# Kernel optimization log

Hardware: AMD Instinct MI355X
Metric: run time of the kernel (lower is better)

The kernel has to match this reference:

```python
import jax, jax.numpy as jnp
import numpy as np

B, D, E, H, K = 8192, 1024, 8, 4096, 2

def setup_inputs() -> dict:
    key = jax.random.key(0)
    ks = jax.random.split(key, 7)
    s_in = 1.0 / np.sqrt(D)
    s_hid = 1.0 / np.sqrt(H)
    return {
        "z":  jax.random.normal(ks[0], (B, D), dtype=jnp.float32),
        "Wg": jax.random.uniform(ks[1], (D, E), jnp.float32, -s_in, s_in),
        "bg": jnp.zeros((E,), jnp.float32),
        "W1": jax.random.uniform(ks[2], (E, D, H), jnp.float32, -s_in, s_in),
        "b1": jax.random.uniform(ks[3], (E, H), jnp.float32, -s_in, s_in),
        "W2": jax.random.uniform(ks[4], (E, H, D), jnp.float32, -s_hid, s_hid),
        "b2": jax.random.uniform(ks[5], (E, D), jnp.float32, -s_hid, s_hid),
    }

def reference(z, Wg, bg, W1, b1, W2, b2):
    # gate: softmax over experts, then keep only top-k weights (no renorm,
    # matching the original which sums topw * expert(z))
    w = jax.nn.softmax(z @ Wg + bg, axis=-1)            # [B, E]
    topw, idx = jax.lax.top_k(w, K)                      # [B, K] each
    wmask = jnp.zeros_like(w).at[jnp.arange(B)[:, None], idx].set(topw)  # [B, E]
    # dense all-expert MLP, then weighted combine (same math as per-token loop)
    h = jax.nn.relu(jnp.einsum('bd,edh->beh', z, W1) + b1)   # [B, E, H]
    y = jnp.einsum('beh,ehd->bed', h, W2) + b2               # [B, E, D]
    out = jnp.einsum('be,bed->bd', wmask, y)                 # [B, D]
    return out
```

## Files before the change

### kernel.cpp

```cpp
#include <hip/hip_runtime.h>
#include <hip/hip_bf16.h>
#include <cstdint>
#include <cstddef>

#define BTOK  8192
#define DIM   1024
#define NEXP  8
#define NHID  4096
#define HHALF 2048
#define GATE_TOK 64
#define ABASE (128 * 32)

typedef __bf16 bf16x8 __attribute__((ext_vector_type(8)));
typedef float  floatx4 __attribute__((ext_vector_type(4)));

#define O_COUNTS 0
#define O_BASE   256
#define O_TOKB   1024
#define O_TOKW   (O_TOKB + (size_t)NEXP*BTOK*4)
#define O_CE     (O_TOKW + (size_t)NEXP*BTOK*4)
#define O_CP     (O_CE + (size_t)2*BTOK*4)
#define O_CW     (O_CP + (size_t)2*BTOK*4)
#define O_ZBF    (O_CW + (size_t)2*BTOK*4)
#define O_W1T    (O_ZBF + (size_t)BTOK*DIM*2)
#define O_W2T    (O_W1T + (size_t)NEXP*DIM*NHID*2)
#define O_HBUF   (O_W2T + (size_t)NEXP*DIM*NHID*2)
#define WS_BASE  (O_HBUF + (size_t)2*BTOK*HHALF*2)
#define O_YBUF   WS_BASE
#define WS_FULL  (O_YBUF + (size_t)2*BTOK*DIM*4)

__device__ __forceinline__ void gload_lds16(const void* g, void* l) {
  __builtin_amdgcn_global_load_lds(
      (const __attribute__((address_space(1))) void*)g,
      (__attribute__((address_space(3))) void*)l, 16, 0, 0);
}

__device__ __forceinline__ ushort f2bf(float x) {
  return __builtin_bit_cast(ushort, __float2bfloat16(x));
}

__global__ void k_zcnt(int* __restrict__ counts) {
  if (threadIdx.x < 12) counts[threadIdx.x] = 0;
}

__global__ void k_zout(float* __restrict__ out) {
  int i = blockIdx.x * blockDim.x + threadIdx.x;
  float4 z4 = {0.f, 0.f, 0.f, 0.f};
  float4* o = (float4*)out;
  int n = BTOK * DIM / 4;
  for (int j = i; j < n; j += gridDim.x * blockDim.x) o[j] = z4;
}

__global__ __launch_bounds__(256) void k_transpose(
    const float* __restrict__ src, __hip_bfloat16* __restrict__ dst, int R, int C) {
  __shared__ float tile[32][33];
  int zz = blockIdx.z;
  const float* s = src + (size_t)zz * R * C;
  __hip_bfloat16* d = dst + (size_t)zz * R * C;
  int c0 = blockIdx.x * 32, r0 = blockIdx.y * 32;
  int tx = threadIdx.x & 31, ty = threadIdx.x >> 5;
#pragma unroll
  for (int i = ty; i < 32; i += 8)
    tile[i][tx] = s[(size_t)(r0 + i) * C + c0 + tx];
  __syncthreads();
#pragma unroll
  for (int i = ty; i < 32; i += 8)
    d[(size_t)(c0 + i) * R + r0 + tx] = __float2bfloat16(tile[tx][i]);
}

__global__ __launch_bounds__(256) void k_gate(
    const float* __restrict__ z, const float* __restrict__ Wg,
    const float* __restrict__ bg, int* __restrict__ counts,
    int* __restrict__ tokb, float* __restrict__ tokw,
    int* __restrict__ ce, int* __restrict__ cp, float* __restrict__ cw,
    __hip_bfloat16* __restrict__ zbf) {
  __shared__ float wgT[NEXP * DIM];
  __shared__ int   le[2 * GATE_TOK];
  __shared__ float lw[2 * GATE_TOK];
  __shared__ int   lr[2 * GATE_TOK];
  __shared__ int   lcnt[NEXP];
  __shared__ int   gbase[NEXP];

  int tid = threadIdx.x;
  if (tid < NEXP) lcnt[tid] = 0;
#pragma unroll
  for (int e = 0; e < NEXP; e++)
    for (int d = tid; d < DIM; d += 256)
      wgT[e * DIM + d] = Wg[d * NEXP + e];
  __syncthreads();

  int lane = tid & 63;
  int wv = tid >> 6;
  int b0 = blockIdx.x * GATE_TOK;

  for (int t = 0; t < 16; t++) {
    int lt = wv * 16 + t;
    int b = b0 + lt;
    const float4* zr4 = (const float4*)(z + (size_t)b * DIM);
    float4 zv[4];
#pragma unroll
    for (int i = 0; i < 4; i++) zv[i] = zr4[lane + 64 * i];
    ushort4* zb4 = (ushort4*)((ushort*)zbf + (size_t)b * DIM);
#pragma unroll
    for (int i = 0; i < 4; i++) {
      ushort4 u;
      u.x = f2bf(zv[i].x); u.y = f2bf(zv[i].y);
      u.z = f2bf(zv[i].z); u.w = f2bf(zv[i].w);
      zb4[lane + 64 * i] = u;
    }
    float acc[NEXP];
#pragma unroll
    for (int e = 0; e < NEXP; e++) acc[e] = 0.f;
#pragma unroll
    for (int e = 0; e < NEXP; e++) {
      const float4* wg4 = (const float4*)(wgT + e * DIM);
#pragma unroll
      for (int i = 0; i < 4; i++) {
        float4 w4 = wg4[lane + 64 * i];
        acc[e] += zv[i].x * w4.x + zv[i].y * w4.y + zv[i].z * w4.z + zv[i].w * w4.w;
      }
    }
#pragma unroll
    for (int off = 32; off > 0; off >>= 1) {
#pragma unroll
      for (int e = 0; e < NEXP; e++) acc[e] += __shfl_down(acc[e], off);
    }
    if (lane == 0) {
      float mx = -1e30f;
#pragma unroll
      for (int e = 0; e < NEXP; e++) { acc[e] += bg[e]; mx = fmaxf(mx, acc[e]); }
      float s = 0.f;
#pragma unroll
      for (int e = 0; e < NEXP; e++) { acc[e] = expf(acc[e] - mx); s += acc[e]; }
      float inv = 1.f / s;
      int i1 = -1, i2 = -1; float v1 = -1.f, v2 = -1.f;
#pragma unroll
      for (int e = 0; e < NEXP; e++) {
        float w = acc[e] * inv;
        if (w > v1) { v2 = v1; i2 = i1; v1 = w; i1 = e; }
        else if (w > v2) { v2 = w; i2 = e; }
      }
      le[2 * lt] = i1;     lw[2 * lt] = v1;
      le[2 * lt + 1] = i2; lw[2 * lt + 1] = v2;
    }
  }
  __syncthreads();
  if (tid < 2 * GATE_TOK) lr[tid] = atomicAdd(&lcnt[le[tid]], 1);
  __syncthreads();
  if (tid < NEXP) gbase[tid] = atomicAdd(&counts[tid], lcnt[tid]);
  __syncthreads();
  if (tid < 2 * GATE_TOK) {
    int e = le[tid];
    int p = gbase[e] + lr[tid];
    int b = b0 + (tid >> 1);
    int slot = tid & 1;
    tokb[e * BTOK + p] = b;
    tokw[e * BTOK + p] = lw[tid];
    ce[2 * b + slot] = e;
    cp[2 * b + slot] = p;
    cw[2 * b + slot] = lw[tid];
  }
}

__global__ void k_base(const int* __restrict__ counts, int* __restrict__ base) {
  if (threadIdx.x == 0 && blockIdx.x == 0) {
    int s = 0;
    for (int e = 0; e < NEXP; e++) { base[e] = s; s += counts[e]; }
    int a = 0, b = 0;
    base[8] = 0; base[17] = 0;
    for (int e = 0; e < NEXP; e++) {
      int mt = (counts[e] + 127) >> 7;
      a += mt * 8; b += mt * 4;
      base[9 + e] = a; base[18 + e] = b;
    }
  }
}


#define STG3(nxt_, tt_) do {                                                 \
    gload_lds16(srcA  + (tt_) * 32, &lds[nxt_][(wv * 16) * 32]);             \
    gload_lds16(srcB0 + (tt_) * 32, &lds[nxt_][ABASE + (wv * 16) * 32]);     \
    gload_lds16(srcB1 + (tt_) * 32, &lds[nxt_][ABASE + (128 + wv * 16) * 32]);\
  } while (0)

#define PH3(cur_, STG_, VM_) do {                                            \
    const ushort* Ab_ = &lds[cur_][0];                                       \
    const ushort* Bb_ = &lds[cur_][ABASE];                                   \
    bf16x8 afr_[4], bfr_[4];                                                 \
    _Pragma("unroll")                                                        \
    for (int j_ = 0; j_ < 4; j_++)                                           \
      bfr_[j_] = __builtin_bit_cast(bf16x8,                                  \
          *(const uint4*)(Bb_ + boff + j_ * 512));                           \
    _Pragma("unroll")                                                        \
    for (int i_ = 0; i_ < 4; i_++)                                           \
      afr_[i_] = __builtin_bit_cast(bf16x8,                                  \
          *(const uint4*)(Ab_ + aoff + i_ * 512));                           \
    STG_;                                                                    \
    __builtin_amdgcn_sched_barrier(0);                                       \
    VM_;                                                                     \
    __builtin_amdgcn_s_barrier();                                            \
    __builtin_amdgcn_sched_barrier(0);                                       \
    __builtin_amdgcn_s_setprio(1);                                           \
    _Pragma("unroll")                                                        \
    for (int i_ = 0; i_ < 4; i_++)                                           \
      _Pragma("unroll")                                                      \
      for (int j_ = 0; j_ < 4; j_++)                                         \
        acc[i_][j_] = __builtin_amdgcn_mfma_f32_16x16x32_bf16(               \
            afr_[i_], bfr_[j_], acc[i_][j_], 0, 0, 0);                       \
    __builtin_amdgcn_s_setprio(0);                                           \
    __builtin_amdgcn_sched_barrier(0);                                       \
    __builtin_amdgcn_s_barrier();                                            \
  } while (0)

#define VM3  asm volatile("s_waitcnt vmcnt(3)" ::: "memory")
#define VM0  asm volatile("s_waitcnt vmcnt(0)" ::: "memory")
#define NOP_ (void)0

__global__ __launch_bounds__(512, 4) void k_gemm1(
    const __hip_bfloat16* __restrict__ zbf, const __hip_bfloat16* __restrict__ w1t,
    const float* __restrict__ b1, const int* __restrict__ counts,
    const int* __restrict__ base, const int* __restrict__ tokb,
    __hip_bfloat16* __restrict__ hbuf, int hbase,
    const int* __restrict__ tp, int* __restrict__ steal) {
  __shared__ __align__(16) ushort lds[3][(128 + 256) * 32];
  __shared__ int sh_g;

  int tid = threadIdx.x;
  int lane = tid & 63;
  int wv = tid >> 6;
  int wm = wv >> 2;
  int wn = wv & 3;
  int lrow = lane & 15;
  int quad = lane >> 4;
  int pc = quad ^ ((lrow >> 1) & 3);
  int aoff = (wm * 64 + lrow) * 32 + pc * 8;
  int boff = (wn * 64 + lrow) * 32 + pc * 8;
  int srow = wv * 16 + (lane >> 2);
  int sswz = ((lane & 3) ^ ((srow >> 1) & 3)) * 8;

  const ushort* zb = (const ushort*)zbf;
  const ushort* w1 = (const ushort*)w1t;
  const int NT = DIM / 32;
  int TT = tp[8];

  for (;;) {
    if (tid == 0) sh_g = atomicAdd(steal, 1);
    __syncthreads();
    int g = sh_g;
    if (g >= TT) break;

    int e = 0;
    while (g >= tp[e + 1]) e++;
    int local = g - tp[e];
    int mte = (tp[e + 1] - tp[e]) >> 3;
    int nt = local / mte;
    int mtl = local - nt * mte;
    int m0 = mtl * 128, n0 = nt * 256;
    int cnt = counts[e], gb = base[e];

    int m = m0 + srow; if (m >= cnt) m = cnt - 1;
    const ushort* srcA = zb + (size_t)tokb[e * BTOK + m] * DIM + sswz;
    const ushort* srcB0 = w1 + (size_t)(e * NHID + hbase + n0 + srow) * DIM + sswz;
    const ushort* srcB1 = w1 + (size_t)(e * NHID + hbase + n0 + 128 + srow) * DIM + sswz;

    STG3(0, 0);
    STG3(1, 1);
    VM3;
    __builtin_amdgcn_s_barrier();

    floatx4 acc[4][4];
#pragma unroll
    for (int i = 0; i < 4; i++)
#pragma unroll
      for (int j = 0; j < 4; j++) { floatx4 zf = {0.f,0.f,0.f,0.f}; acc[i][j] = zf; }

    int cur = 0;
#pragma unroll 1
    for (int t = 0; t < NT - 2; ++t) {
      int nxt = cur + 2; if (nxt >= 3) nxt -= 3;
      PH3(cur, STG3(nxt, t + 2), VM3);
      cur = (cur == 2) ? 0 : cur + 1;
    }
    PH3(cur, NOP_, VM0);
    cur = (cur == 2) ? 0 : cur + 1;
    PH3(cur, NOP_, NOP_);

    float bias[4];
#pragma unroll
    for (int j = 0; j < 4; j++)
      bias[j] = b1[e * NHID + hbase + n0 + wn * 64 + j * 16 + lrow];
    ushort* hp = (ushort*)hbuf;
#pragma unroll
    for (int i = 0; i < 4; i++) {
      int mloc = wm * 64 + i * 16 + quad * 4;
#pragma unroll
      for (int r = 0; r < 4; r++) {
        int mm = m0 + mloc + r;
        if (mm < cnt) {
          ushort* hr = hp + (size_t)(gb + mm) * HHALF;
#pragma unroll
          for (int j = 0; j < 4; j++) {
            float v = fmaxf(acc[i][j][r] + bias[j], 0.f);
            hr[n0 + wn * 64 + j * 16 + lrow] = f2bf(v);
          }
        }
      }
    }
    __syncthreads();
  }
}

__global__ __launch_bounds__(512, 4) void k_gemm2(
    const __hip_bfloat16* __restrict__ hbuf, const __hip_bfloat16* __restrict__ w2t,
    const float* __restrict__ b2, const int* __restrict__ counts,
    const int* __restrict__ base, const int* __restrict__ tokb,
    const float* __restrict__ tokw, float* __restrict__ out,
    float* __restrict__ ybuf, int hbase, int pass,
    const int* __restrict__ tp, int* __restrict__ steal) {
  __shared__ __align__(16) ushort lds[3][(128 + 256) * 32];
  __shared__ int sh_g;

  int tid = threadIdx.x;
  int lane = tid & 63;
  int wv = tid >> 6;
  int wm = wv >> 2;
  int wn = wv & 3;
  int lrow = lane & 15;
  int quad = lane >> 4;
  int pc = quad ^ ((lrow >> 1) & 3);
  int aoff = (wm * 64 + lrow) * 32 + pc * 8;
  int boff = (wn * 64 + lrow) * 32 + pc * 8;
  int srow = wv * 16 + (lane >> 2);
  int sswz = ((lane & 3) ^ ((srow >> 1) & 3)) * 8;

  const ushort* hb = (const ushort*)hbuf;
  const ushort* w2 = (const ushort*)w2t;
  const int NT = HHALF / 32;
  int TT = tp[8];

  for (;;) {
    if (tid == 0) sh_g = atomicAdd(steal, 1);
    __syncthreads();
    int g = sh_g;
    if (g >= TT) break;

    int e = 0;
    while (g >= tp[e + 1]) e++;
    int local = g - tp[e];
    int mte = (tp[e + 1] - tp[e]) >> 2;
    int nt = local / mte;
    int mtl = local - nt * mte;
    int m0 = mtl * 128, n0 = nt * 256;
    int cnt = counts[e], gb = base[e];

    int m = m0 + srow; if (m >= cnt) m = cnt - 1;
    const ushort* srcA = hb + (size_t)(gb + m) * HHALF + sswz;
    const ushort* srcB0 = w2 + (size_t)(e * DIM + n0 + srow) * NHID + hbase + sswz;
    const ushort* srcB1 = w2 + (size_t)(e * DIM + n0 + 128 + srow) * NHID + hbase + sswz;

    STG3(0, 0);
    STG3(1, 1);
    VM3;
    __builtin_amdgcn_s_barrier();

    floatx4 acc[4][4];
#pragma unroll
    for (int i = 0; i < 4; i++)
#pragma unroll
      for (int j = 0; j < 4; j++) { floatx4 zf = {0.f,0.f,0.f,0.f}; acc[i][j] = zf; }

    int cur = 0;
#pragma unroll 1
    for (int t = 0; t < NT - 2; ++t) {
      int nxt = cur + 2; if (nxt >= 3) nxt -= 3;
      PH3(cur, STG3(nxt, t + 2), VM3);
      cur = (cur == 2) ? 0 : cur + 1;
    }
    PH3(cur, NOP_, VM0);
    cur = (cur == 2) ? 0 : cur + 1;
    PH3(cur, NOP_, NOP_);

    if (ybuf) {
      float bias[4];
#pragma unroll
      for (int j = 0; j < 4; j++)
        bias[j] = pass ? b2[e * DIM + n0 + wn * 64 + j * 16 + lrow] : 0.f;
#pragma unroll
      for (int i = 0; i < 4; i++) {
        int mloc = wm * 64 + i * 16 + quad * 4;
#pragma unroll
        for (int r = 0; r < 4; r++) {
          int mm = m0 + mloc + r;
          if (mm < cnt) {
            float* yr = ybuf + (size_t)(gb + mm) * DIM;
#pragma unroll
            for (int j = 0; j < 4; j++) {
              int n = n0 + wn * 64 + j * 16 + lrow;
              if (pass == 0) yr[n] = acc[i][j][r];
              else           yr[n] += acc[i][j][r] + bias[j];
            }
          }
        }
      }
    } else {
#pragma unroll
      for (int i = 0; i < 4; i++) {
        int mloc = wm * 64 + i * 16 + quad * 4;
#pragma unroll
        for (int r = 0; r < 4; r++) {
          int mm = m0 + mloc + r;
          if (mm < cnt) {
            int tk  = tokb[e * BTOK + mm];
            float w = tokw[e * BTOK + mm];
#pragma unroll
            for (int j = 0; j < 4; j++) {
              int n = n0 + wn * 64 + j * 16 + lrow;
              float v = acc[i][j][r] + (pass ? b2[e * DIM + n] : 0.f);
              atomicAdd(&out[(size_t)tk * DIM + n], w * v);
            }
          }
        }
      }
    }
    __syncthreads();
  }
}

__global__ __launch_bounds__(256) void k_combine(
    const float* __restrict__ ybuf, const int* __restrict__ base,
    const int* __restrict__ ce, const int* __restrict__ cp,
    const float* __restrict__ cw, float* __restrict__ out) {
  int b = blockIdx.x;
  int n = threadIdx.x * 4;
  int e1 = ce[2 * b], e2 = ce[2 * b + 1];
  int s1 = base[e1] + cp[2 * b];
  int s2 = base[e2] + cp[2 * b + 1];
  float w1 = cw[2 * b], w2 = cw[2 * b + 1];
  float4 a = *(const float4*)(ybuf + (size_t)s1 * DIM + n);
  float4 c = *(const float4*)(ybuf + (size_t)s2 * DIM + n);
  float4 o;
  o.x = w1 * a.x + w2 * c.x;
  o.y = w1 * a.y + w2 * c.y;
  o.z = w1 * a.z + w2 * c.z;
  o.w = w1 * a.w + w2 * c.w;
  *(float4*)(out + (size_t)b * DIM + n) = o;
}

extern "C" void kernel_launch(void* const* d_in, const int* in_sizes, int n_in,
                              void* d_out, int out_size, void* d_ws, size_t ws_size,
                              hipStream_t stream) {
  const float* z  = (const float*)d_in[0];
  const float* Wg = (const float*)d_in[1];
  const float* bg = (const float*)d_in[2];
  const float* W1 = (const float*)d_in[3];
  const float* b1 = (const float*)d_in[4];
  const float* W2 = (const float*)d_in[5];
  const float* b2 = (const float*)d_in[6];
  float* out = (float*)d_out;
  char* ws = (char*)d_ws;
  if (ws_size < WS_BASE) return;
  bool use_ybuf = ws_size >= WS_FULL;

  int*   counts = (int*)(ws + O_COUNTS);
  int*   base   = (int*)(ws + O_BASE);
  int*   tokb   = (int*)(ws + O_TOKB);
  float* tokw   = (float*)(ws + O_TOKW);
  int*   ce     = (int*)(ws + O_CE);
  int*   cp     = (int*)(ws + O_CP);
  float* cw     = (float*)(ws + O_CW);
  __hip_bfloat16* zbf  = (__hip_bfloat16*)(ws + O_ZBF);
  __hip_bfloat16* w1t  = (__hip_bfloat16*)(ws + O_W1T);
  __hip_bfloat16* w2t  = (__hip_bfloat16*)(ws + O_W2T);
  __hip_bfloat16* hbuf = (__hip_bfloat16*)(ws + O_HBUF);
  float* ybuf = use_ybuf ? (float*)(ws + O_YBUF) : nullptr;

  k_zcnt<<<1, 64, 0, stream>>>(counts);
  if (!use_ybuf) k_zout<<<512, 256, 0, stream>>>(out);
  k_transpose<<<dim3(NHID / 32, DIM / 32, NEXP), 256, 0, stream>>>(W1, w1t, DIM, NHID);
  k_transpose<<<dim3(DIM / 32, NHID / 32, NEXP), 256, 0, stream>>>(W2, w2t, NHID, DIM);
  k_gate<<<BTOK / GATE_TOK, 256, 0, stream>>>(z, Wg, bg, counts, tokb, tokw, ce, cp, cw, zbf);
  k_base<<<1, 64, 0, stream>>>(counts, base);
  for (int half = 0; half < 2; half++) {
    k_gemm1<<<512, 512, 0, stream>>>(
        zbf, w1t, b1, counts, base, tokb, hbuf, half * HHALF,
        base + 8, counts + 8 + half * 2);
    k_gemm2<<<512, 512, 0, stream>>>(
        hbuf, w2t, b2, counts, base, tokb, tokw, out, ybuf, half * HHALF, half,
        base + 17, counts + 9 + half * 2);
  }
  if (use_ybuf)
    k_combine<<<BTOK, 256, 0, stream>>>(ybuf, base, ce, cp, cw, out);
}
```

Measured before the change: 913.5 us.

## Replace work-stealing GEMM2 with stream-K split and atomic scatter output

The second expert GEMM now splits the total K-iteration space evenly across the grid (stream-K style), so each block processes a contiguous range of k-steps that may span partial tiles, and accumulates partial results with atomicAdd into the output. The ybuf intermediate path and the separate combine kernel are removed, along with the gate's per-token slot bookkeeping, so the output is always zeroed and scatter-added. The aim is to fix tail imbalance across tiles and drop the extra y-buffer traffic and combine launch, at the cost of more atomic adds to the output and partial-tile reloads.

```diff
diff --git a/kernel.cpp b/kernel.cpp
--- a/kernel.cpp
+++ b/kernel.cpp
@@ -26,8 +26,6 @@
 #define O_W2T    (O_W1T + (size_t)NEXP*DIM*NHID*2)
 #define O_HBUF   (O_W2T + (size_t)NEXP*DIM*NHID*2)
 #define WS_BASE  (O_HBUF + (size_t)2*BTOK*HHALF*2)
-#define O_YBUF   WS_BASE
-#define WS_FULL  (O_YBUF + (size_t)2*BTOK*DIM*4)
 
 __device__ __forceinline__ void gload_lds16(const void* g, void* l) {
   __builtin_amdgcn_global_load_lds(
@@ -72,7 +70,6 @@
     const float* __restrict__ z, const float* __restrict__ Wg,
     const float* __restrict__ bg, int* __restrict__ counts,
     int* __restrict__ tokb, float* __restrict__ tokw,
-    int* __restrict__ ce, int* __restrict__ cp, float* __restrict__ cw,
     __hip_bfloat16* __restrict__ zbf) {
   __shared__ float wgT[NEXP * DIM];
   __shared__ int   le[2 * GATE_TOK];
@@ -153,12 +150,8 @@
     int e = le[tid];
     int p = gbase[e] + lr[tid];
     int b = b0 + (tid >> 1);
-    int slot = tid & 1;
     tokb[e * BTOK + p] = b;
     tokw[e * BTOK + p] = lw[tid];
-    ce[2 * b + slot] = e;
-    cp[2 * b + slot] = p;
-    cw[2 * b + slot] = lw[tid];
   }
 }
 
@@ -315,10 +308,8 @@
     const float* __restrict__ b2, const int* __restrict__ counts,
     const int* __restrict__ base, const int* __restrict__ tokb,
     const float* __restrict__ tokw, float* __restrict__ out,
-    float* __restrict__ ybuf, int hbase, int pass,
-    const int* __restrict__ tp, int* __restrict__ steal) {
+    int hbase, int pass, const int* __restrict__ tp) {
   __shared__ __align__(16) ushort lds[3][(128 + 256) * 32];
-  __shared__ int sh_g;
 
   int tid = threadIdx.x;
   int lane = tid & 63;
@@ -336,13 +327,18 @@
   const ushort* hb = (const ushort*)hbuf;
   const ushort* w2 = (const ushort*)w2t;
   const int NT = HHALF / 32;
+
   int TT = tp[8];
-
-  for (;;) {
-    if (tid == 0) sh_g = atomicAdd(steal, 1);
-    __syncthreads();
-    int g = sh_g;
-    if (g >= TT) break;
+  int totalU = TT * NT;
+  int q = (totalU + (int)gridDim.x - 1) / (int)gridDim.x;
+  int u  = (int)blockIdx.x * q;
+  int u1 = u + q; if (u1 > totalU) u1 = totalU;
+
+  while (u < u1) {
+    int g = u / NT;
+    int ks0 = u - g * NT;
+    int nk = NT - ks0;
+    if (nk > u1 - u) nk = u1 - u;
 
     int e = 0;
     while (g >= tp[e + 1]) e++;
@@ -358,9 +354,9 @@
     const ushort* srcB0 = w2 + (size_t)(e * DIM + n0 + srow) * NHID + hbase + sswz;
     const ushort* srcB1 = w2 + (size_t)(e * DIM + n0 + 128 + srow) * NHID + hbase + sswz;
 
-    STG3(0, 0);
-    STG3(1, 1);
-    VM3;
+    STG3(0, ks0);
+    if (nk > 1) { STG3(1, ks0 + 1); VM3; }
+    else        { VM0; }
     __builtin_amdgcn_s_barrier();
 
     floatx4 acc[4][4];
@@ -371,79 +367,38 @@
 
     int cur = 0;
 #pragma unroll 1
-    for (int t = 0; t < NT - 2; ++t) {
+    for (int t = 0; t < nk - 2; ++t) {
       int nxt = cur + 2; if (nxt >= 3) nxt -= 3;
-      PH3(cur, STG3(nxt, t + 2), VM3);
+      PH3(cur, STG3(nxt, ks0 + t + 2), VM3);
       cur = (cur == 2) ? 0 : cur + 1;
     }
-    PH3(cur, NOP_, VM0);
-    cur = (cur == 2) ? 0 : cur + 1;
+    if (nk > 1) {
+      PH3(cur, NOP_, VM0);
+      cur = (cur == 2) ? 0 : cur + 1;
+    }
     PH3(cur, NOP_, NOP_);
 
-    if (ybuf) {
-      float bias[4];
-#pragma unroll
-      for (int j = 0; j < 4; j++)
-        bias[j] = pass ? b2[e * DIM + n0 + wn * 64 + j * 16 + lrow] : 0.f;
-#pragma unroll
-      for (int i = 0; i < 4; i++) {
-        int mloc = wm * 64 + i * 16 + quad * 4;
-#pragma unroll
-        for (int r = 0; r < 4; r++) {
-          int mm = m0 + mloc + r;
-          if (mm < cnt) {
-            float* yr = ybuf + (size_t)(gb + mm) * DIM;
-#pragma unroll
-            for (int j = 0; j < 4; j++) {
-              int n = n0 + wn * 64 + j * 16 + lrow;
-              if (pass == 0) yr[n] = acc[i][j][r];
-              else           yr[n] += acc[i][j][r] + bias[j];
-            }
+    bool addb2 = (pass == 0) && (ks0 == 0);
+#pragma unroll
+    for (int i = 0; i < 4; i++) {
+      int mloc = wm * 64 + i * 16 + quad * 4;
+#pragma unroll
+      for (int r = 0; r < 4; r++) {
+        int mm = m0 + mloc + r;
+        if (mm < cnt) {
+          int tk  = tokb[e * BTOK + mm];
+          float w = tokw[e * BTOK + mm];
+#pragma unroll
+          for (int j = 0; j < 4; j++) {
+            int n = n0 + wn * 64 + j * 16 + lrow;
+            float v = acc[i][j][r] + (addb2 ? b2[e * DIM + n] : 0.f);
+            atomicAdd(&out[(size_t)tk * DIM + n], w * v);
           }
         }
       }
-    } else {
-#pragma unroll
-      for (int i = 0; i < 4; i++) {
-        int mloc = wm * 64 + i * 16 + quad * 4;
-#pragma unroll
-        for (int r = 0; r < 4; r++) {
-          int mm = m0 + mloc + r;
-          if (mm < cnt) {
-            int tk  = tokb[e * BTOK + mm];
-            float w = tokw[e * BTOK + mm];
-#pragma unroll
-            for (int j = 0; j < 4; j++) {
-              int n = n0 + wn * 64 + j * 16 + lrow;
-              float v = acc[i][j][r] + (pass ? b2[e * DIM + n] : 0.f);
-              atomicAdd(&out[(size_t)tk * DIM + n], w * v);
-            }
-          }
-        }
-      }
-    }
-    __syncthreads();
-  }
-}
-
-__global__ __launch_bounds__(256) void k_combine(
-    const float* __restrict__ ybuf, const int* __restrict__ base,
-    const int* __restrict__ ce, const int* __restrict__ cp,
-    const float* __restrict__ cw, float* __restrict__ out) {
-  int b = blockIdx.x;
-  int n = threadIdx.x * 4;
-  int e1 = ce[2 * b], e2 = ce[2 * b + 1];
-  int s1 = base[e1] + cp[2 * b];
-  int s2 = base[e2] + cp[2 * b + 1];
-  float w1 = cw[2 * b], w2 = cw[2 * b + 1];
-  float4 a = *(const float4*)(ybuf + (size_t)s1 * DIM + n);
-  float4 c = *(const float4*)(ybuf + (size_t)s2 * DIM + n);
-  float4 o;
-  o.x = w1 * a.x + w2 * c.x;
-  o.y = w1 * a.y + w2 * c.y;
-  o.z = w1 * a.z + w2 * c.z;
-  o.w = w1 * a.w + w2 * c.w;
-  *(float4*)(out + (size_t)b * DIM + n) = o;
+    }
+    u += nk;
+  }
 }
 
 extern "C" void kernel_launch(void* const* d_in, const int* in_sizes, int n_in,
@@ -459,35 +414,28 @@
   float* out = (float*)d_out;
   char* ws = (char*)d_ws;
   if (ws_size < WS_BASE) return;
-  bool use_ybuf = ws_size >= WS_FULL;
 
   int*   counts = (int*)(ws + O_COUNTS);
   int*   base   = (int*)(ws + O_BASE);
   int*   tokb   = (int*)(ws + O_TOKB);
   float* tokw   = (float*)(ws + O_TOKW);
-  int*   ce     = (int*)(ws + O_CE);
-  int*   cp     = (int*)(ws + O_CP);
-  float* cw     = (float*)(ws + O_CW);
   __hip_bfloat16* zbf  = (__hip_bfloat16*)(ws + O_ZBF);
   __hip_bfloat16* w1t  = (__hip_bfloat16*)(ws + O_W1T);
   __hip_bfloat16* w2t  = (__hip_bfloat16*)(ws + O_W2T);
   __hip_bfloat16* hbuf = (__hip_bfloat16*)(ws + O_HBUF);
-  float* ybuf = use_ybuf ? (float*)(ws + O_YBUF) : nullptr;
 
   k_zcnt<<<1, 64, 0, stream>>>(counts);
-  if (!use_ybuf) k_zout<<<512, 256, 0, stream>>>(out);
+  k_zout<<<512, 256, 0, stream>>>(out);
   k_transpose<<<dim3(NHID / 32, DIM / 32, NEXP), 256, 0, stream>>>(W1, w1t, DIM, NHID);
   k_transpose<<<dim3(DIM / 32, NHID / 32, NEXP), 256, 0, stream>>>(W2, w2t, NHID, DIM);
-  k_gate<<<BTOK / GATE_TOK, 256, 0, stream>>>(z, Wg, bg, counts, tokb, tokw, ce, cp, cw, zbf);
+  k_gate<<<BTOK / GATE_TOK, 256, 0, stream>>>(z, Wg, bg, counts, tokb, tokw, zbf);
   k_base<<<1, 64, 0, stream>>>(counts, base);
   for (int half = 0; half < 2; half++) {
     k_gemm1<<<512, 512, 0, stream>>>(
         zbf, w1t, b1, counts, base, tokb, hbuf, half * HHALF,
         base + 8, counts + 8 + half * 2);
     k_gemm2<<<512, 512, 0, stream>>>(
-        hbuf, w2t, b2, counts, base, tokb, tokw, out, ybuf, half * HHALF, half,
-        base + 17, counts + 9 + half * 2);
-  }
-  if (use_ybuf)
-    k_combine<<<BTOK, 256, 0, stream>>>(ybuf, base, ce, cp, cw, out);
-}
+        hbuf, w2t, b2, counts, base, tokb, tokw, out,
+        half * HHALF, half, base + 17);
+  }
+}
```

After: 1.005 ms. 1.1x slower.

## Shrink GEMM tiles to 128x128 with 256-thread blocks and more resident blocks

Applied to the files above, without the earlier changes.

Both expert GEMM kernels move from 128x256 output tiles computed by 8 waves to 128x128 tiles computed by 4 waves, each wave still producing a 64x64 sub-tile. Staging now issues four 16-byte loads per thread per K-step (two A halves, two B halves), and the wait count and tile-count bookkeeping in k_base are updated to match. The persistent grid grows to 768 blocks with launch bounds of 256 threads and 3 blocks per CU. The aim is more tiles for better load balance and smaller LDS per block, at the cost of less reuse of each loaded A and B tile and more total global traffic.

```diff
diff --git a/kernel.cpp b/kernel.cpp
--- a/kernel.cpp
+++ b/kernel.cpp
@@ -170,17 +170,18 @@
     base[8] = 0; base[17] = 0;
     for (int e = 0; e < NEXP; e++) {
       int mt = (counts[e] + 127) >> 7;
-      a += mt * 8; b += mt * 4;
+      a += mt * 16; b += mt * 8;
       base[9 + e] = a; base[18 + e] = b;
     }
   }
 }
 
 
-#define STG3(nxt_, tt_) do {                                                 \
-    gload_lds16(srcA  + (tt_) * 32, &lds[nxt_][(wv * 16) * 32]);             \
-    gload_lds16(srcB0 + (tt_) * 32, &lds[nxt_][ABASE + (wv * 16) * 32]);     \
-    gload_lds16(srcB1 + (tt_) * 32, &lds[nxt_][ABASE + (128 + wv * 16) * 32]);\
+#define STG4(nxt_, tt_) do {                                                  \
+    gload_lds16(srcA0 + (tt_) * 32, &lds[nxt_][(wv * 16) * 32]);              \
+    gload_lds16(srcA1 + (tt_) * 32, &lds[nxt_][(64 + wv * 16) * 32]);         \
+    gload_lds16(srcB0 + (tt_) * 32, &lds[nxt_][ABASE + (wv * 16) * 32]);      \
+    gload_lds16(srcB1 + (tt_) * 32, &lds[nxt_][ABASE + (64 + wv * 16) * 32]); \
   } while (0)
 
 #define PH3(cur_, STG_, VM_) do {                                            \
@@ -212,24 +213,24 @@
     __builtin_amdgcn_s_barrier();                                            \
   } while (0)
 
-#define VM3  asm volatile("s_waitcnt vmcnt(3)" ::: "memory")
+#define VM4  asm volatile("s_waitcnt vmcnt(4)" ::: "memory")
 #define VM0  asm volatile("s_waitcnt vmcnt(0)" ::: "memory")
 #define NOP_ (void)0
 
-__global__ __launch_bounds__(512, 4) void k_gemm1(
+__global__ __launch_bounds__(256, 3) void k_gemm1(
     const __hip_bfloat16* __restrict__ zbf, const __hip_bfloat16* __restrict__ w1t,
     const float* __restrict__ b1, const int* __restrict__ counts,
     const int* __restrict__ base, const int* __restrict__ tokb,
     __hip_bfloat16* __restrict__ hbuf, int hbase,
     const int* __restrict__ tp, int* __restrict__ steal) {
-  __shared__ __align__(16) ushort lds[3][(128 + 256) * 32];
+  __shared__ __align__(16) ushort lds[3][(128 + 128) * 32];
   __shared__ int sh_g;
 
   int tid = threadIdx.x;
   int lane = tid & 63;
   int wv = tid >> 6;
-  int wm = wv >> 2;
-  int wn = wv & 3;
+  int wm = wv >> 1;
+  int wn = wv & 1;
   int lrow = lane & 15;
   int quad = lane >> 4;
   int pc = quad ^ ((lrow >> 1) & 3);
@@ -252,20 +253,22 @@
     int e = 0;
     while (g >= tp[e + 1]) e++;
     int local = g - tp[e];
-    int mte = (tp[e + 1] - tp[e]) >> 3;
+    int mte = (tp[e + 1] - tp[e]) >> 4;
     int nt = local / mte;
     int mtl = local - nt * mte;
-    int m0 = mtl * 128, n0 = nt * 256;
+    int m0 = mtl * 128, n0 = nt * 128;
     int cnt = counts[e], gb = base[e];
 
-    int m = m0 + srow; if (m >= cnt) m = cnt - 1;
-    const ushort* srcA = zb + (size_t)tokb[e * BTOK + m] * DIM + sswz;
+    int ma = m0 + srow;      if (ma >= cnt) ma = cnt - 1;
+    int mb = m0 + 64 + srow; if (mb >= cnt) mb = cnt - 1;
+    const ushort* srcA0 = zb + (size_t)tokb[e * BTOK + ma] * DIM + sswz;
+    const ushort* srcA1 = zb + (size_t)tokb[e * BTOK + mb] * DIM + sswz;
     const ushort* srcB0 = w1 + (size_t)(e * NHID + hbase + n0 + srow) * DIM + sswz;
-    const ushort* srcB1 = w1 + (size_t)(e * NHID + hbase + n0 + 128 + srow) * DIM + sswz;
-
-    STG3(0, 0);
-    STG3(1, 1);
-    VM3;
+    const ushort* srcB1 = w1 + (size_t)(e * NHID + hbase + n0 + 64 + srow) * DIM + sswz;
+
+    STG4(0, 0);
+    STG4(1, 1);
+    VM4;
     __builtin_amdgcn_s_barrier();
 
     floatx4 acc[4][4];
@@ -278,7 +281,7 @@
 #pragma unroll 1
     for (int t = 0; t < NT - 2; ++t) {
       int nxt = cur + 2; if (nxt >= 3) nxt -= 3;
-      PH3(cur, STG3(nxt, t + 2), VM3);
+      PH3(cur, STG4(nxt, t + 2), VM4);
       cur = (cur == 2) ? 0 : cur + 1;
     }
     PH3(cur, NOP_, VM0);
@@ -310,21 +313,21 @@
   }
 }
 
-__global__ __launch_bounds__(512, 4) void k_gemm2(
+__global__ __launch_bounds__(256, 3) void k_gemm2(
     const __hip_bfloat16* __restrict__ hbuf, const __hip_bfloat16* __restrict__ w2t,
     const float* __restrict__ b2, const int* __restrict__ counts,
     const int* __restrict__ base, const int* __restrict__ tokb,
     const float* __restrict__ tokw, float* __restrict__ out,
     float* __restrict__ ybuf, int hbase, int pass,
     const int* __restrict__ tp, int* __restrict__ steal) {
-  __shared__ __align__(16) ushort lds[3][(128 + 256) * 32];
+  __shared__ __align__(16) ushort lds[3][(128 + 128) * 32];
   __shared__ int sh_g;
 
   int tid = threadIdx.x;
   int lane = tid & 63;
   int wv = tid >> 6;
-  int wm = wv >> 2;
-  int wn = wv & 3;
+  int wm = wv >> 1;
+  int wn = wv & 1;
   int lrow = lane & 15;
   int quad = lane >> 4;
   int pc = quad ^ ((lrow >> 1) & 3);
@@ -347,20 +350,22 @@
     int e = 0;
     while (g >= tp[e + 1]) e++;
     int local = g - tp[e];
-    int mte = (tp[e + 1] - tp[e]) >> 2;
+    int mte = (tp[e + 1] - tp[e]) >> 3;
     int nt = local / mte;
     int mtl = local - nt * mte;
-    int m0 = mtl * 128, n0 = nt * 256;
+    int m0 = mtl * 128, n0 = nt * 128;
     int cnt = counts[e], gb = base[e];
 
-    int m = m0 + srow; if (m >= cnt) m = cnt - 1;
-    const ushort* srcA = hb + (size_t)(gb + m) * HHALF + sswz;
+    int ma = m0 + srow;      if (ma >= cnt) ma = cnt - 1;
+    int mb = m0 + 64 + srow; if (mb >= cnt) mb = cnt - 1;
+    const ushort* srcA0 = hb + (size_t)(gb + ma) * HHALF + sswz;
+    const ushort* srcA1 = hb + (size_t)(gb + mb) * HHALF + sswz;
     const ushort* srcB0 = w2 + (size_t)(e * DIM + n0 + srow) * NHID + hbase + sswz;
-    const ushort* srcB1 = w2 + (size_t)(e * DIM + n0 + 128 + srow) * NHID + hbase + sswz;
-
-    STG3(0, 0);
-    STG3(1, 1);
-    VM3;
+    const ushort* srcB1 = w2 + (size_t)(e * DIM + n0 + 64 + srow) * NHID + hbase + sswz;
+
+    STG4(0, 0);
+    STG4(1, 1);
+    VM4;
     __builtin_amdgcn_s_barrier();
 
     floatx4 acc[4][4];
@@ -373,7 +378,7 @@
 #pragma unroll 1
     for (int t = 0; t < NT - 2; ++t) {
       int nxt = cur + 2; if (nxt >= 3) nxt -= 3;
-      PH3(cur, STG3(nxt, t + 2), VM3);
+      PH3(cur, STG4(nxt, t + 2), VM4);
       cur = (cur == 2) ? 0 : cur + 1;
     }
     PH3(cur, NOP_, VM0);
@@ -481,10 +486,10 @@
   k_gate<<<BTOK / GATE_TOK, 256, 0, stream>>>(z, Wg, bg, counts, tokb, tokw, ce, cp, cw, zbf);
   k_base<<<1, 64, 0, stream>>>(counts, base);
   for (int half = 0; half < 2; half++) {
-    k_gemm1<<<512, 512, 0, stream>>>(
+    k_gemm1<<<768, 256, 0, stream>>>(
         zbf, w1t, b1, counts, base, tokb, hbuf, half * HHALF,
         base + 8, counts + 8 + half * 2);
-    k_gemm2<<<512, 512, 0, stream>>>(
+    k_gemm2<<<768, 256, 0, stream>>>(
         hbuf, w2t, b2, counts, base, tokb, tokw, out, ybuf, half * HHALF, half,
         base + 17, counts + 9 + half * 2);
   }
```

New measurement: 932.7 us. 1.02x slower.
